# Kernel optimization log

Measured on AMD Instinct MI355X. Metric: run time of the kernel, lower is better.

The kernel has to match this reference:

```python
import jax, jax.numpy as jnp
import numpy as np

V = 50000
E = 800000
HIDDEN = 128
NUM_BASES = 64
D_MIN, D_MAX = 0.0, 25.0  # squared-distance range for radius=5.0


def setup_inputs() -> dict:
    key = jax.random.key(0)
    ks = jax.random.split(key, 10)
    s = 1.0 / np.sqrt(HIDDEN)
    sb = 1.0 / np.sqrt(NUM_BASES)
    return {
        "X": jax.random.normal(ks[0], (V, HIDDEN), jnp.float32),
        "R": jax.random.normal(ks[1], (V, 3), jnp.float32),
        "src": jax.random.randint(ks[2], (E,), 0, V),
        "dest": jax.random.randint(ks[3], (E,), 0, V),
        # filter-generating MLP (no bias, per nn.Linear(..., bias=False))
        "W1": jax.random.uniform(ks[4], (NUM_BASES, HIDDEN), jnp.float32, -sb, sb),
        "W2": jax.random.uniform(ks[5], (HIDDEN, HIDDEN), jnp.float32, -s, s),
        # update MLP (with bias)
        "U1": jax.random.uniform(ks[6], (HIDDEN, HIDDEN), jnp.float32, -s, s),
        "b1": jax.random.uniform(ks[7], (HIDDEN,), jnp.float32, -s, s),
        "U2": jax.random.uniform(ks[8], (HIDDEN, HIDDEN), jnp.float32, -s, s),
        "b2": jax.random.uniform(ks[9], (HIDDEN,), jnp.float32, -s, s),
    }


def _rbf(d):
    # Gaussian RBF expansion: centers linspaced over [D_MIN, D_MAX]
    centers = jnp.linspace(D_MIN, D_MAX, NUM_BASES, dtype=d.dtype)
    width = (D_MAX - D_MIN) / (NUM_BASES - 1)
    return jnp.exp(-((d[:, None] - centers) ** 2) / (2.0 * width * width))  # [E, num_bases]


def reference(X, R, src, dest, W1, W2, U1, b1, U2, b2):
    # squared pairwise distance per edge (original: .square().sum(-1), no sqrt)
    D_ij = jnp.sum((R[src] - R[dest]) ** 2, axis=-1)  # [E]
    # filter-generating network: RBF -> Linear -> ReLU -> Linear -> ReLU
    M = jax.nn.relu(_rbf(D_ij) @ W1)
    M = jax.nn.relu(M @ W2)  # [E, d_h]
    # gather-multiply-scatter: continuous-filter convolution
    H = jax.ops.segment_sum(X[src] * M, dest, num_segments=X.shape[0])  # [V, d_h]
    # update MLP (note: self.W(X) in the original is dead code, overwritten)
    out = jax.nn.relu(H @ U1 + b1) @ U2 + b2
    return out
```

## Files before the change

kernel.cpp:

```cpp
#include <hip/hip_runtime.h>
#include <hip/hip_bf16.h>
#include <hip/hip_fp16.h>

#define HIDDEN 128
#define NB 64
#define TG 8192
#define TPTS (TG + 1)
#define TMAX 32.0f
#define TINV ((float)TG / TMAX)
#define CAP 64
#define NB1 1024
#define BINCAP 20

typedef _Float16 f16;
typedef _Float16 f16x8 __attribute__((ext_vector_type(8)));
typedef float floatx4 __attribute__((ext_vector_type(4)));
typedef unsigned short ushort;
typedef unsigned int uint;

__global__ __launch_bounds__(256) void megaprep(
    const int* __restrict__ src, const int* __restrict__ dest,
    const float* __restrict__ R, float4* __restrict__ Rp,
    const float* __restrict__ X, f16* __restrict__ Xh,
    const float* __restrict__ W1, const float* __restrict__ W2,
    f16* __restrict__ Th,
    const float* __restrict__ U1, const float* __restrict__ U2,
    f16* __restrict__ U1p, f16* __restrict__ U2p,
    uint* __restrict__ staging, uint* __restrict__ cnt1,
    int E, int V, int XB, int TB, int RB, int EPB) {
    __shared__ uint smem[256 + 256 * BINCAP];
    const int b = blockIdx.x;
    const int tid = threadIdx.x;
    if (b < NB1) {
        uint* scur = smem;
        uint* sbin = smem + 256;
        scur[tid] = 0;
        __syncthreads();
        const int e0 = b * EPB;
        const int e1 = min(e0 + EPB, E);
        for (int e = e0 + tid; e < e1; e += 256) {
            const uint s = (uint)src[e];
            const uint d = (uint)dest[e];
            const uint bin = d >> 8;
            const uint k = atomicAdd(&scur[bin], 1u);
            if (k < BINCAP) sbin[bin * BINCAP + k] = s | ((d & 255u) << 16);
        }
        __syncthreads();
        const uint n = min(scur[tid], (uint)BINCAP);
        uint4* dst = (uint4*)(staging + ((size_t)b * 256 + tid) * BINCAP);
        const uint4* sp = (const uint4*)(sbin + tid * BINCAP);
        for (uint k4 = 0; k4 * 4 < n; ++k4) dst[k4] = sp[k4];
        cnt1[b * 256 + tid] = n;
    } else if (b < NB1 + XB) {
        const int idx = ((b - NB1) * 256 + tid) * 8;
        if (idx < V * HIDDEN) {
            const float4 v0 = *(const float4*)(X + idx);
            const float4 v1 = *(const float4*)(X + idx + 4);
            f16x8 h;
            h[0] = (f16)v0.x; h[1] = (f16)v0.y; h[2] = (f16)v0.z; h[3] = (f16)v0.w;
            h[4] = (f16)v1.x; h[5] = (f16)v1.y; h[6] = (f16)v1.z; h[7] = (f16)v1.w;
            *(f16x8*)(Xh + idx) = h;
        }
    } else if (b < NB1 + XB + TB) {
        f16* h2 = (f16*)smem;
        const int lane = tid & 63;
        const int w = tid >> 6;
        const int rt = w & 1;
        const int ct0 = (w >> 1) * 4;
        const int lrow = lane & 15;
        const int lk = lane >> 4;
        const int g0 = (b - NB1 - XB) * 32;
        const float d2a = (float)(g0 + rt * 16 + lrow) * (TMAX / (float)TG);
        const float wid = 25.0f / 63.0f;
        f16x8 a[4];
#pragma unroll
        for (int kt = 0; kt < 2; ++kt)
#pragma unroll
            for (int j = 0; j < 8; ++j) {
                const float z = d2a - wid * (float)(kt * 32 + lk * 8 + j);
                a[kt][j] = (f16)expf(-(z * z) / (2.0f * wid * wid));
            }
        floatx4 acc[4];
#pragma unroll
        for (int c = 0; c < 4; ++c) acc[c] = (floatx4){0.f, 0.f, 0.f, 0.f};
#pragma unroll
        for (int c = 0; c < 4; ++c) {
            const int col = (ct0 + c) * 16 + lrow;
#pragma unroll
            for (int kt = 0; kt < 2; ++kt) {
                f16x8 bf;
#pragma unroll
                for (int j = 0; j < 8; ++j)
                    bf[j] = (f16)W1[(kt * 32 + lk * 8 + j) * HIDDEN + col];
                acc[c] = __builtin_amdgcn_mfma_f32_16x16x32_f16(a[kt], bf, acc[c], 0, 0, 0);
            }
        }
#pragma unroll
        for (int c = 0; c < 4; ++c) {
            const int col = (ct0 + c) * 16 + lrow;
#pragma unroll
            for (int rr = 0; rr < 4; ++rr)
                h2[(rt * 16 + lk * 4 + rr) * 136 + col] = (f16)fmaxf(acc[c][rr], 0.0f);
        }
        __syncthreads();
        f16x8 a2[4];
#pragma unroll
        for (int kt = 0; kt < 4; ++kt)
            a2[kt] = *(const f16x8*)&h2[(rt * 16 + lrow) * 136 + kt * 32 + lk * 8];
#pragma unroll
        for (int c = 0; c < 4; ++c) acc[c] = (floatx4){0.f, 0.f, 0.f, 0.f};
#pragma unroll
        for (int c = 0; c < 4; ++c) {
            const int col = (ct0 + c) * 16 + lrow;
#pragma unroll
            for (int kt = 0; kt < 4; ++kt) {
                f16x8 bf;
#pragma unroll
                for (int j = 0; j < 8; ++j)
                    bf[j] = (f16)W2[(kt * 32 + lk * 8 + j) * HIDDEN + col];
                acc[c] = __builtin_amdgcn_mfma_f32_16x16x32_f16(a2[kt], bf, acc[c], 0, 0, 0);
            }
        }
#pragma unroll
        for (int c = 0; c < 4; ++c) {
            const int col = (ct0 + c) * 16 + lrow;
#pragma unroll
            for (int rr = 0; rr < 4; ++rr) {
                const int g = g0 + rt * 16 + lk * 4 + rr;
                if (g <= TG) Th[(size_t)g * 128 + col] = (f16)fmaxf(acc[c][rr], 0.0f);
            }
        }
    } else if (b < NB1 + XB + TB + RB) {
        const int v = (b - NB1 - XB - TB) * 256 + tid;
        if (v < V) Rp[v] = make_float4(R[3 * v], R[3 * v + 1], R[3 * v + 2], 0.f);
    } else {
        const int ub = b - NB1 - XB - TB - RB;
        const int i = (ub & 63) * 256 + tid;
        const int j = i & 7;
        const int l = (i >> 3) & 63;
        const int ktct = i >> 9;
        const int kt = ktct >> 3, ct = ktct & 7;
        const int srcidx = (kt * 32 + (l >> 4) * 8 + j) * HIDDEN + ct * 16 + (l & 15);
        if (ub < 64) U1p[i] = (f16)U1[srcidx];
        else         U2p[i] = (f16)U2[srcidx];
    }
}

__global__ __launch_bounds__(256) void bucketize(
    const uint* __restrict__ staging, const uint* __restrict__ cnt1,
    ushort* __restrict__ eps, int* __restrict__ deg, int V) {
    __shared__ ushort bucket[256 * CAP];
    __shared__ uint lcur[256];
    const int r = blockIdx.x;
    const int tid = threadIdx.x;
    lcur[tid] = 0;
    __syncthreads();
    for (int b = tid; b < NB1; b += 256) {
        uint n = cnt1[b * 256 + r];
        n = min(n, (uint)BINCAP);
        const uint* seg = staging + ((size_t)b * 256 + r) * BINCAP;
        for (uint k = 0; k < n; ++k) {
            const uint e = seg[k];
            const uint dl = e >> 16;
            const uint kk = atomicAdd(&lcur[dl], 1u);
            if (kk < CAP) bucket[dl * CAP + kk] = (ushort)(e & 0xFFFFu);
        }
    }
    __syncthreads();
    const uint4* bs = (const uint4*)bucket;
    uint4* ed = (uint4*)(eps + (size_t)r * (256 * CAP));
    for (int i = tid; i < 256 * CAP / 8; i += 256) ed[i] = bs[i];
    const int d = r * 256 + tid;
    if (d < V) deg[d] = (int)min(lcur[tid], (uint)CAP);
}

__global__ __launch_bounds__(1024) void gather_mlp(
    const int* __restrict__ deg, const ushort* __restrict__ eps,
    const float4* __restrict__ Rp,
    const f16* __restrict__ Xh, const f16* __restrict__ Th,
    const f16x8* __restrict__ U1p, const float* __restrict__ b1,
    const f16x8* __restrict__ U2p, const float* __restrict__ b2,
    float* __restrict__ out, int V) {
    __shared__ f16 hg[16 * 136];
    __shared__ f16 h2[16 * 136];
    const int tid = threadIdx.x;
    const int lane = tid & 63;
    const int wid = tid >> 6;
    const int nb = blockIdx.x * 16;

    {
        const int cl = lane & 15;
        const int es = lane >> 4;
        const char* thb = (const char*)Th + cl * 16;
        const char* xhb = (const char*)Xh + cl * 16;
        const int node = nb + wid;
        const int dn = (node < V) ? deg[node] : 0;
        const float4 rn = Rp[min(node, V - 1)];
        float acc[8];
#pragma unroll
        for (int i = 0; i < 8; ++i) acc[i] = 0.0f;
        int my_s = 0;
        if (lane < dn) my_s = (int)eps[((size_t)node << 6) + lane];
        const float4 rs = Rp[my_s];
        const float dx = rs.x - rn.x;
        const float dy = rs.y - rn.y;
        const float dz = rs.z - rn.z;
        const float D2 = fmaf(dx, dx, fmaf(dy, dy, dz * dz));
        const int my_g = (lane < dn) ? min((int)fmaf(D2, TINV, 0.5f), TG) : TG;
        const int nst2 = (((dn + 3) >> 2) + 1) & ~1;
        for (int j = 0; j < nst2; j += 2) {
            const int idx0 = 4 * j + es;
            const int idx1 = idx0 + 4;
            const int s0 = __shfl(my_s, idx0);
            const int g0 = __shfl(my_g, idx0);
            const int s1 = __shfl(my_s, idx1);
            const int g1 = __shfl(my_g, idx1);
            const f16x8 m0 = *(const f16x8*)(thb + g0 * 256);
            const f16x8 x0 = *(const f16x8*)(xhb + s0 * 256);
            const f16x8 m1 = *(const f16x8*)(thb + g1 * 256);
            const f16x8 x1 = *(const f16x8*)(xhb + s1 * 256);
#pragma unroll
            for (int i = 0; i < 8; ++i)
                acc[i] = fmaf((float)m0[i], (float)x0[i], acc[i]);
#pragma unroll
            for (int i = 0; i < 8; ++i)
                acc[i] = fmaf((float)m1[i], (float)x1[i], acc[i]);
        }
#pragma unroll
        for (int i = 0; i < 8; ++i) {
            acc[i] += __shfl_xor(acc[i], 16);
            acc[i] += __shfl_xor(acc[i], 32);
        }
        if (es == 0) {
            f16x8 h;
#pragma unroll
            for (int i = 0; i < 8; ++i) h[i] = (f16)acc[i];
            *(f16x8*)&hg[wid * 136 + cl * 8] = h;
        }
    }
    __syncthreads();

    const int lrow = lane & 15;
    const int lk = lane >> 4;
    if (wid < 8) {
        const int ct = wid;
        f16x8 a[4];
#pragma unroll
        for (int kt = 0; kt < 4; ++kt)
            a[kt] = *(const f16x8*)&hg[lrow * 136 + kt * 32 + lk * 8];
        floatx4 acc = (floatx4){0.f, 0.f, 0.f, 0.f};
#pragma unroll
        for (int kt = 0; kt < 4; ++kt) {
            const f16x8 bf = U1p[(kt * 8 + ct) * 64 + lane];
            acc = __builtin_amdgcn_mfma_f32_16x16x32_f16(a[kt], bf, acc, 0, 0, 0);
        }
        const int col = ct * 16 + lrow;
        const float bb = b1[col];
#pragma unroll
        for (int rr = 0; rr < 4; ++rr)
            h2[(lk * 4 + rr) * 136 + col] = (f16)fmaxf(acc[rr] + bb, 0.0f);
    }
    __syncthreads();
    if (wid < 8) {
        const int ct = wid;
        f16x8 a[4];
#pragma unroll
        for (int kt = 0; kt < 4; ++kt)
            a[kt] = *(const f16x8*)&h2[lrow * 136 + kt * 32 + lk * 8];
        floatx4 acc = (floatx4){0.f, 0.f, 0.f, 0.f};
#pragma unroll
        for (int kt = 0; kt < 4; ++kt) {
            const f16x8 bf = U2p[(kt * 8 + ct) * 64 + lane];
            acc = __builtin_amdgcn_mfma_f32_16x16x32_f16(a[kt], bf, acc, 0, 0, 0);
        }
        const int col = ct * 16 + lrow;
        const float bb = b2[col];
#pragma unroll
        for (int rr = 0; rr < 4; ++rr) {
            const int row = nb + lk * 4 + rr;
            if (row < V) out[(size_t)row * HIDDEN + col] = acc[rr] + bb;
        }
    }
}

extern "C" void kernel_launch(void* const* d_in, const int* in_sizes, int n_in,
                              void* d_out, int out_size, void* d_ws, size_t ws_size,
                              hipStream_t stream) {
    const float* X = (const float*)d_in[0];
    const float* R = (const float*)d_in[1];
    const int* src = (const int*)d_in[2];
    const int* dest = (const int*)d_in[3];
    const float* W1 = (const float*)d_in[4];
    const float* W2 = (const float*)d_in[5];
    const float* U1 = (const float*)d_in[6];
    const float* b1 = (const float*)d_in[7];
    const float* U2 = (const float*)d_in[8];
    const float* b2 = (const float*)d_in[9];

    const int V = in_sizes[0] / HIDDEN;
    const int E = in_sizes[2];
    const int XB = (V * HIDDEN / 8 + 255) / 256;
    const int TB = (TPTS + 31) / 32;
    const int RB = (V + 255) / 256;
    const int NR = (V + 255) >> 8;
    const int EPB = (E + NB1 - 1) / NB1;

    char* base = (char*)d_ws;
    f16* Th = (f16*)base;                       base += ((size_t)TPTS * 128 * sizeof(f16) + 255) & ~255;
    f16* Xh = (f16*)base;                       base += (size_t)V * HIDDEN * sizeof(f16);
    ushort* eps = (ushort*)base;                base += (size_t)NR * 256 * CAP * sizeof(ushort);
    float4* Rp = (float4*)base;                 base += (size_t)V * sizeof(float4);
    f16* U1p = (f16*)base;                      base += (size_t)HIDDEN * HIDDEN * sizeof(f16);
    f16* U2p = (f16*)base;                      base += (size_t)HIDDEN * HIDDEN * sizeof(f16);
    uint* staging = (uint*)base;                base += (size_t)NB1 * 256 * BINCAP * sizeof(uint);
    uint* cnt1 = (uint*)base;                   base += (size_t)NB1 * 256 * sizeof(uint);
    int* deg = (int*)base;                      base += (size_t)NR * 256 * sizeof(int);

    megaprep<<<NB1 + XB + TB + RB + 128, 256, 0, stream>>>(
        src, dest, R, Rp, X, Xh, W1, W2, Th, U1, U2, U1p, U2p,
        staging, cnt1, E, V, XB, TB, RB, EPB);
    bucketize<<<NR, 256, 0, stream>>>(staging, cnt1, eps, deg, V);
    gather_mlp<<<(V + 15) / 16, 1024, 0, stream>>>(deg, eps, (const float4*)Rp,
                                                   Xh, Th, (const f16x8*)U1p, b1,
                                                   (const f16x8*)U2p, b2,
                                                   (float*)d_out, V);
}
```

Baseline: 94.63 us.

## Process 64 nodes per block with LDS atomic work-stealing across waves

Each 1024-thread block of the gather/MLP kernel now covers 64 nodes instead of 16. Its 16 waves claim nodes dynamically through a shared-memory atomic counter, which balances the uneven per-node degree. The update MLP now runs on all 16 waves over four row tiles, so every wave issues MFMA work where only 8 did before, and U1/U2 fragment loads are amortised over more rows. In exchange the block count drops by four, the LDS footprint per block grows, and the counter atomics add some latency.

```diff
diff --git a/kernel.cpp b/kernel.cpp
--- a/kernel.cpp
+++ b/kernel.cpp
@@ -181,73 +181,86 @@
     const f16x8* __restrict__ U1p, const float* __restrict__ b1,
     const f16x8* __restrict__ U2p, const float* __restrict__ b2,
     float* __restrict__ out, int V) {
-    __shared__ f16 hg[16 * 136];
-    __shared__ f16 h2[16 * 136];
+    __shared__ f16 hg[64 * 136];
+    __shared__ f16 h2[64 * 136];
+    __shared__ uint ctr;
     const int tid = threadIdx.x;
     const int lane = tid & 63;
     const int wid = tid >> 6;
-    const int nb = blockIdx.x * 16;
+    const int nb = blockIdx.x * 64;
+
+    if (tid == 0) ctr = 0;
+    __syncthreads();
 
     {
         const int cl = lane & 15;
         const int es = lane >> 4;
         const char* thb = (const char*)Th + cl * 16;
         const char* xhb = (const char*)Xh + cl * 16;
-        const int node = nb + wid;
-        const int dn = (node < V) ? deg[node] : 0;
-        const float4 rn = Rp[min(node, V - 1)];
-        float acc[8];
-#pragma unroll
-        for (int i = 0; i < 8; ++i) acc[i] = 0.0f;
-        int my_s = 0;
-        if (lane < dn) my_s = (int)eps[((size_t)node << 6) + lane];
-        const float4 rs = Rp[my_s];
-        const float dx = rs.x - rn.x;
-        const float dy = rs.y - rn.y;
-        const float dz = rs.z - rn.z;
-        const float D2 = fmaf(dx, dx, fmaf(dy, dy, dz * dz));
-        const int my_g = (lane < dn) ? min((int)fmaf(D2, TINV, 0.5f), TG) : TG;
-        const int nst2 = (((dn + 3) >> 2) + 1) & ~1;
-        for (int j = 0; j < nst2; j += 2) {
-            const int idx0 = 4 * j + es;
-            const int idx1 = idx0 + 4;
-            const int s0 = __shfl(my_s, idx0);
-            const int g0 = __shfl(my_g, idx0);
-            const int s1 = __shfl(my_s, idx1);
-            const int g1 = __shfl(my_g, idx1);
-            const f16x8 m0 = *(const f16x8*)(thb + g0 * 256);
-            const f16x8 x0 = *(const f16x8*)(xhb + s0 * 256);
-            const f16x8 m1 = *(const f16x8*)(thb + g1 * 256);
-            const f16x8 x1 = *(const f16x8*)(xhb + s1 * 256);
-#pragma unroll
-            for (int i = 0; i < 8; ++i)
-                acc[i] = fmaf((float)m0[i], (float)x0[i], acc[i]);
-#pragma unroll
-            for (int i = 0; i < 8; ++i)
-                acc[i] = fmaf((float)m1[i], (float)x1[i], acc[i]);
-        }
-#pragma unroll
-        for (int i = 0; i < 8; ++i) {
-            acc[i] += __shfl_xor(acc[i], 16);
-            acc[i] += __shfl_xor(acc[i], 32);
-        }
-        if (es == 0) {
-            f16x8 h;
-#pragma unroll
-            for (int i = 0; i < 8; ++i) h[i] = (f16)acc[i];
-            *(f16x8*)&hg[wid * 136 + cl * 8] = h;
+        for (;;) {
+            uint nloc = 0;
+            if (lane == 0) nloc = atomicAdd(&ctr, 1u);
+            nloc = (uint)__shfl((int)nloc, 0);
+            if (nloc >= 64u) break;
+            const int node = nb + (int)nloc;
+            const int dn = (node < V) ? deg[node] : 0;
+            const float4 rn = Rp[min(node, V - 1)];
+            float acc[8];
+#pragma unroll
+            for (int i = 0; i < 8; ++i) acc[i] = 0.0f;
+            int my_s = 0;
+            if (lane < dn) my_s = (int)eps[((size_t)node << 6) + lane];
+            const float4 rs = Rp[my_s];
+            const float dx = rs.x - rn.x;
+            const float dy = rs.y - rn.y;
+            const float dz = rs.z - rn.z;
+            const float D2 = fmaf(dx, dx, fmaf(dy, dy, dz * dz));
+            const int my_g = (lane < dn) ? min((int)fmaf(D2, TINV, 0.5f), TG) : TG;
+            const int nst2 = (((dn + 3) >> 2) + 1) & ~1;
+            for (int j = 0; j < nst2; j += 2) {
+                const int idx0 = 4 * j + es;
+                const int idx1 = idx0 + 4;
+                const int s0 = __shfl(my_s, idx0);
+                const int g0 = __shfl(my_g, idx0);
+                const int s1 = __shfl(my_s, idx1);
+                const int g1 = __shfl(my_g, idx1);
+                const f16x8 m0 = *(const f16x8*)(thb + g0 * 256);
+                const f16x8 x0 = *(const f16x8*)(xhb + s0 * 256);
+                const f16x8 m1 = *(const f16x8*)(thb + g1 * 256);
+                const f16x8 x1 = *(const f16x8*)(xhb + s1 * 256);
+#pragma unroll
+                for (int i = 0; i < 8; ++i)
+                    acc[i] = fmaf((float)m0[i], (float)x0[i], acc[i]);
+#pragma unroll
+                for (int i = 0; i < 8; ++i)
+                    acc[i] = fmaf((float)m1[i], (float)x1[i], acc[i]);
+            }
+#pragma unroll
+            for (int i = 0; i < 8; ++i) {
+                acc[i] += __shfl_xor(acc[i], 16);
+                acc[i] += __shfl_xor(acc[i], 32);
+            }
+            if (es == 0) {
+                f16x8 h;
+#pragma unroll
+                for (int i = 0; i < 8; ++i) h[i] = (f16)acc[i];
+                *(f16x8*)&hg[(int)nloc * 136 + cl * 8] = h;
+            }
         }
     }
     __syncthreads();
 
     const int lrow = lane & 15;
     const int lk = lane >> 4;
-    if (wid < 8) {
-        const int ct = wid;
+#pragma unroll
+    for (int t = 0; t < 2; ++t) {
+        const int tile = wid + t * 16;
+        const int rt = tile & 3;
+        const int ct = tile >> 2;
         f16x8 a[4];
 #pragma unroll
         for (int kt = 0; kt < 4; ++kt)
-            a[kt] = *(const f16x8*)&hg[lrow * 136 + kt * 32 + lk * 8];
+            a[kt] = *(const f16x8*)&hg[(rt * 16 + lrow) * 136 + kt * 32 + lk * 8];
         floatx4 acc = (floatx4){0.f, 0.f, 0.f, 0.f};
 #pragma unroll
         for (int kt = 0; kt < 4; ++kt) {
@@ -258,15 +271,18 @@
         const float bb = b1[col];
 #pragma unroll
         for (int rr = 0; rr < 4; ++rr)
-            h2[(lk * 4 + rr) * 136 + col] = (f16)fmaxf(acc[rr] + bb, 0.0f);
-    }
-    __syncthreads();
-    if (wid < 8) {
-        const int ct = wid;
+            h2[(rt * 16 + lk * 4 + rr) * 136 + col] = (f16)fmaxf(acc[rr] + bb, 0.0f);
+    }
+    __syncthreads();
+#pragma unroll
+    for (int t = 0; t < 2; ++t) {
+        const int tile = wid + t * 16;
+        const int rt = tile & 3;
+        const int ct = tile >> 2;
         f16x8 a[4];
 #pragma unroll
         for (int kt = 0; kt < 4; ++kt)
-            a[kt] = *(const f16x8*)&h2[lrow * 136 + kt * 32 + lk * 8];
+            a[kt] = *(const f16x8*)&h2[(rt * 16 + lrow) * 136 + kt * 32 + lk * 8];
         floatx4 acc = (floatx4){0.f, 0.f, 0.f, 0.f};
 #pragma unroll
         for (int kt = 0; kt < 4; ++kt) {
@@ -277,7 +293,7 @@
         const float bb = b2[col];
 #pragma unroll
         for (int rr = 0; rr < 4; ++rr) {
-            const int row = nb + lk * 4 + rr;
+            const int row = nb + rt * 16 + lk * 4 + rr;
             if (row < V) out[(size_t)row * HIDDEN + col] = acc[rr] + bb;
         }
     }
@@ -320,7 +336,7 @@
         src, dest, R, Rp, X, Xh, W1, W2, Th, U1, U2, U1p, U2p,
         staging, cnt1, E, V, XB, TB, RB, EPB);
     bucketize<<<NR, 256, 0, stream>>>(staging, cnt1, eps, deg, V);
-    gather_mlp<<<(V + 15) / 16, 1024, 0, stream>>>(deg, eps, (const float4*)Rp,
+    gather_mlp<<<(V + 63) / 64, 1024, 0, stream>>>(deg, eps, (const float4*)Rp,
                                                    Xh, Th, (const f16x8*)U1p, b1,
                                                    (const f16x8*)U2p, b2,
                                                    (float*)d_out, V);
```

After: 95.69 us. About the same (+1.1%).
